# Optimization experiments

Measured on AMD Instinct MI355X. Metric: run time of the kernel, lower is better.

## Reference

```python
import jax, jax.numpy as jnp
import numpy as np

EPS = 1e-5

def conv1x1(x, w, b):
    # x: [B,Cin,H,W], w: [Cout,Cin], b: [Cout]
    return jnp.einsum('oi,bihw->bohw', w, x) + b[None, :, None, None]

def self_attention(x, qw, qb, kw, kb, vw, vb, fw, fb):
    B, C, H, W = x.shape
    hid = qw.shape[0]
    q = conv1x1(x, qw, qb).reshape(B, hid, H * W).transpose(0, 2, 1)   # [B,HW,hid]
    k = conv1x1(x, kw, kb).reshape(B, hid, H * W)                      # [B,hid,HW]
    v = conv1x1(x, vw, vb).reshape(B, C, H * W)                        # [B,C,HW]
    attn = jax.nn.softmax(jnp.einsum('bnh,bhm->bnm', q, k), axis=-1)   # [B,HW,HW]
    z = jnp.einsum('bnm,bcm->bnc', attn, v)                            # [B,HW,C]
    # faithful to torch .view(B,C,H,W) on contiguous [B,HW,C]: raw reshape, no transpose
    z = z.reshape(B, C, H, W)
    return conv1x1(z * x, fw, fb) + x

def group_norm_per_channel(y, gw, gb):
    # GroupNorm(num_groups == num_channels): per-channel instance norm, biased var
    mean = y.mean(axis=(2, 3), keepdims=True)
    var = ((y - mean) ** 2).mean(axis=(2, 3), keepdims=True)
    yn = (y - mean) * jax.lax.rsqrt(var + EPS)
    return yn * gw[None, :, None, None] + gb[None, :, None, None]

def setup_inputs() -> dict:
    key = jax.random.key(0)
    ks = jax.random.split(key, 32)
    B, C, H, W = 4, 64, 64, 64
    hid, att = 64, 64
    d = {}
    d['x'] = jax.random.normal(ks[0], (B, C, H, W), jnp.float32)
    d['h'] = jax.random.normal(ks[1], (B, hid, H, W), jnp.float32)
    d['c'] = jax.random.normal(ks[2], (B, hid, H, W), jnp.float32)
    i = 3
    for pre, cin in (('ax', C), ('ah', hid)):
        for nm, cout in (('q', att), ('k', att), ('v', cin), ('f', cin)):
            d[f'{pre}_{nm}w'] = jax.random.normal(ks[i], (cout, cin), jnp.float32) * 0.05; i += 1
            d[f'{pre}_{nm}b'] = jax.random.normal(ks[i], (cout,), jnp.float32) * 0.05; i += 1
    d['conv_w'] = jax.random.normal(ks[i], (4 * hid, C + hid, 3, 3), jnp.float32) * 0.05; i += 1
    d['conv_b'] = jax.random.normal(ks[i], (4 * hid,), jnp.float32) * 0.05; i += 1
    d['gn_w'] = jnp.ones((4 * hid,), jnp.float32)
    d['gn_b'] = jnp.zeros((4 * hid,), jnp.float32)
    return d

def reference(x, h, c,
              ax_qw, ax_qb, ax_kw, ax_kb, ax_vw, ax_vb, ax_fw, ax_fb,
              ah_qw, ah_qb, ah_kw, ah_kb, ah_vw, ah_vb, ah_fw, ah_fb,
              conv_w, conv_b, gn_w, gn_b):
    hid = h.shape[1]
    xa = self_attention(x, ax_qw, ax_qb, ax_kw, ax_kb, ax_vw, ax_vb, ax_fw, ax_fb)
    ha = self_attention(h, ah_qw, ah_qb, ah_kw, ah_kb, ah_vw, ah_vb, ah_fw, ah_fb)
    combined = jnp.concatenate([xa, ha], axis=1)
    y = jax.lax.conv_general_dilated(
        combined, conv_w, window_strides=(1, 1), padding=[(1, 1), (1, 1)],
        dimension_numbers=('NCHW', 'OIHW', 'NCHW')) + conv_b[None, :, None, None]
    y = group_norm_per_channel(y, gn_w, gn_b)
    i, f, o, g = jnp.split(y, 4, axis=1)
    i = jax.nn.sigmoid(i); f = jax.nn.sigmoid(f); o = jax.nn.sigmoid(o); g = jnp.tanh(g)
    c_next = f * c + i * g
    h_next = o * jnp.tanh(c_next)
    return jnp.stack([h_next, c_next])  # [2,B,hid,H,W]
```

## Files before the change

### kernel.cpp

```cpp
#include <hip/hip_runtime.h>
#include <hip/hip_bf16.h>


typedef __hip_bfloat16 bf16;
typedef const __hip_bfloat16* bfp;
typedef short bf16x8 __attribute__((ext_vector_type(8)));
typedef short short4v __attribute__((ext_vector_type(4)));
typedef float f32x4 __attribute__((ext_vector_type(4)));
typedef unsigned int u32x4 __attribute__((ext_vector_type(4)));

#define SM_SHIFT 12.0f

__device__ __forceinline__ float ldf(const void* p, long i, int f32) {
    return f32 ? ((const float*)p)[i]
               : __bfloat162float(((const bf16*)p)[i]);
}
__device__ __forceinline__ short f2bf(float f) {
    bf16 h = __float2bfloat16(f);
    return *reinterpret_cast<short*>(&h);
}
__device__ __forceinline__ void xbswap(unsigned& a, unsigned& b, int mask, bool up) {
    unsigned s = up ? a : b;
    unsigned r = __shfl_xor(s, mask, 64);
    a = up ? r : a;
    b = up ? b : r;
}

__device__ __forceinline__ int sniff_f32(const void* xr)
{
    int lane = threadIdx.x & 63;
    unsigned long long v = ((const unsigned long long*)xr)[lane];
    int ok = 0;
#pragma unroll
    for (int i = 0; i < 4; ++i) {
        int e = (int)((v >> (16 * i + 7)) & 0xFF);
        ok += (e >= 100 && e <= 141);
    }
    ok += __shfl_xor(ok, 1, 64);
    ok += __shfl_xor(ok, 2, 64);
    ok += __shfl_xor(ok, 4, 64);
    ok += __shfl_xor(ok, 8, 64);
    ok += __shfl_xor(ok, 16, 64);
    ok += __shfl_xor(ok, 32, 64);
    return ok < 200;
}

__global__ __launch_bounds__(256) void qkv_kernel(
    const void* __restrict__ Xx, const void* __restrict__ Xh,
    const void* __restrict__ qwx, const void* __restrict__ qbx,
    const void* __restrict__ kwx, const void* __restrict__ kbx,
    const void* __restrict__ vwx, const void* __restrict__ vbx,
    const void* __restrict__ qwh, const void* __restrict__ qbh,
    const void* __restrict__ kwh, const void* __restrict__ kbh,
    const void* __restrict__ vwh, const void* __restrict__ vbh,
    bf16* __restrict__ Qx, bf16* __restrict__ Kx, bf16* __restrict__ Vtx,
    bf16* __restrict__ Qh, bf16* __restrict__ Kh, bf16* __restrict__ Vth,
    const void* __restrict__ cw, bf16* __restrict__ Wt,
    float* __restrict__ gacc, int qkvN)
{
    int bx = blockIdx.x;
    int tid = threadIdx.x;
    int f32 = sniff_f32(Xx);
    if (bx >= qkvN) {
        if (bx == qkvN) {
            for (int j = 0; j < 8; ++j)
                gacc[tid * 8 + j] = 0.f;
        }
        int wi = (bx - qkvN) * 256 + tid;
        int tap = wi >> 15;
        int rem = wi & 32767;
        int oc = rem >> 7, ic = rem & 127;
        Wt[wi] = __float2bfloat16(ldf(cw, ((long)oc * 128 + ic) * 9 + tap, f32));
        return;
    }
    __shared__ __align__(16) short xt[64][72];
    __shared__ __align__(16) short wq[64][72];
    __shared__ __align__(16) short wk[64][72];
    __shared__ __align__(16) short wv[64][72];
    int ab  = (bx >> 8) & 1;
    int idx = bx & 255;
    int b = idx >> 6;
    int n0 = (idx & 63) * 64;
    int wave = tid >> 6, lane = tid & 63;
    int q = lane >> 4, l15 = lane & 15;

    const void* X = ab ? Xh : Xx;
    const void* qw = ab ? qwh : qwx; const void* qb = ab ? qbh : qbx;
    const void* kw = ab ? kwh : kwx; const void* kb = ab ? kbh : kbx;
    const void* vw = ab ? vwh : vwx; const void* vb = ab ? vbh : vbx;
    short* Qg  = (short*)(ab ? Qh  : Qx)  + (long)b * 262144;
    short* Kg  = (short*)(ab ? Kh  : Kx)  + (long)b * 262144;
    short* Vtg = (short*)(ab ? Vth : Vtx) + (long)b * 262144;

    if (!f32) {
        const short* q16 = (const short*)qw;
        const short* k16 = (const short*)kw;
        const short* v16 = (const short*)vw;
        for (int rep = 0; rep < 2; ++rep) {
            int j8 = (rep * 256 + tid) * 8;
            *(bf16x8*)&wq[j8 >> 6][j8 & 63] = *(const bf16x8*)(q16 + j8);
            *(bf16x8*)&wk[j8 >> 6][j8 & 63] = *(const bf16x8*)(k16 + j8);
            *(bf16x8*)&wv[j8 >> 6][j8 & 63] = *(const bf16x8*)(v16 + j8);
        }
    } else {
        for (int rep = 0; rep < 16; ++rep) {
            int j = rep * 256 + tid;
            int i = j >> 6, cc = j & 63;
            wq[i][cc] = f2bf(((const float*)qw)[j]);
            wk[i][cc] = f2bf(((const float*)kw)[j]);
            wv[i][cc] = f2bf(((const float*)vw)[j]);
        }
    }
    long xbase = (long)b * 262144;
    for (int rep = 0; rep < 16; ++rep) {
        int c = rep * 4 + (tid >> 6);
        int p = tid & 63;
        xt[p][c] = f2bf(ldf(X, xbase + (long)c * 4096 + n0 + p, f32));
    }
    __syncthreads();

    bf16x8 a0 = *(const bf16x8*)&xt[wave * 16 + l15][q * 8];
    bf16x8 a1 = *(const bf16x8*)&xt[wave * 16 + l15][32 + q * 8];

    for (int ct = 0; ct < 4; ++ct) {
        bf16x8 bq0 = *(const bf16x8*)&wq[ct * 16 + l15][q * 8];
        bf16x8 bq1 = *(const bf16x8*)&wq[ct * 16 + l15][32 + q * 8];
        f32x4 z = (f32x4){0.f, 0.f, 0.f, 0.f};
        z = __builtin_amdgcn_mfma_f32_16x16x32_bf16(a0, bq0, z, 0, 0, 0);
        z = __builtin_amdgcn_mfma_f32_16x16x32_bf16(a1, bq1, z, 0, 0, 0);
        float bias = ldf(qb, ct * 16 + l15, f32);
        for (int reg = 0; reg < 4; ++reg)
            Qg[(long)(n0 + wave * 16 + q * 4 + reg) * 64 + ct * 16 + l15] =
                f2bf(z[reg] + bias);
    }
    for (int ct = 0; ct < 4; ++ct) {
        bf16x8 bk0 = *(const bf16x8*)&wk[ct * 16 + l15][q * 8];
        bf16x8 bk1 = *(const bf16x8*)&wk[ct * 16 + l15][32 + q * 8];
        f32x4 z = (f32x4){0.f, 0.f, 0.f, 0.f};
        z = __builtin_amdgcn_mfma_f32_16x16x32_bf16(a0, bk0, z, 0, 0, 0);
        z = __builtin_amdgcn_mfma_f32_16x16x32_bf16(a1, bk1, z, 0, 0, 0);
        float bias = ldf(kb, ct * 16 + l15, f32);
        for (int reg = 0; reg < 4; ++reg)
            Kg[(long)(n0 + wave * 16 + q * 4 + reg) * 64 + ct * 16 + l15] =
                f2bf(z[reg] + bias);
    }
    bf16x8 av0 = *(const bf16x8*)&wv[wave * 16 + l15][q * 8];
    bf16x8 av1 = *(const bf16x8*)&wv[wave * 16 + l15][32 + q * 8];
    for (int ct = 0; ct < 4; ++ct) {
        bf16x8 bx0 = *(const bf16x8*)&xt[ct * 16 + l15][q * 8];
        bf16x8 bx1 = *(const bf16x8*)&xt[ct * 16 + l15][32 + q * 8];
        f32x4 z = (f32x4){0.f, 0.f, 0.f, 0.f};
        z = __builtin_amdgcn_mfma_f32_16x16x32_bf16(av0, bx0, z, 0, 0, 0);
        z = __builtin_amdgcn_mfma_f32_16x16x32_bf16(av1, bx1, z, 0, 0, 0);
        for (int reg = 0; reg < 4; ++reg) {
            int c_out = wave * 16 + q * 4 + reg;
            float bias = ldf(vb, c_out, f32);
            Vtg[(long)c_out * 4096 + n0 + ct * 16 + l15] = f2bf(z[reg] + bias);
        }
    }
}

__global__ __launch_bounds__(256, 2) void attn_kernel(
    bfp Qx, bfp Kx, bfp Vtx, bf16* Ox,
    bfp Qh, bfp Kh, bfp Vth, bf16* Oh,
    float* __restrict__ lw, int split)
{
    __shared__ __align__(16) short ks [2][64][64];
    __shared__ __align__(16) short vts[2][64][64];
    int tid = threadIdx.x;
    int wave = tid >> 6, lane = tid & 63;
    int q = lane >> 4, l15 = lane & 15;
    int idx = blockIdx.x & 255;
    int ab, half, mstart, ntile;
    if (split) {
        ab = blockIdx.x >> 9; half = (blockIdx.x >> 8) & 1;
        mstart = half * 2048; ntile = 32;
    } else {
        ab = blockIdx.x >> 8; half = 0; mstart = 0; ntile = 64;
    }
    int b = idx >> 6;
    int rt = idx & 63;
    int n0 = rt * 64 + wave * 16;
    const short* Qb  = (const short*)(ab ? Qh  : Qx)  + (long)b * 262144;
    const short* Kb  = (const short*)(ab ? Kh  : Kx)  + (long)b * 262144;
    const short* Vtb = (const short*)(ab ? Vth : Vtx) + (long)b * 262144;
    short* Ob = (short*)(ab ? Oh : Ox) + (long)half * (1l << 20) + (long)b * 262144;

    bf16x8 aq0 = *(const bf16x8*)(Qb + (long)(n0 + l15) * 64 + q * 8);
    bf16x8 aq1 = *(const bf16x8*)(Qb + (long)(n0 + l15) * 64 + 32 + q * 8);

    f32x4 acc_o[4];
    for (int ct = 0; ct < 4; ++ct) acc_o[ct] = (f32x4){0.f, 0.f, 0.f, 0.f};
    float l_acc = 0.f;

    int swp = (l15 >> 1) & 7;
    int c0 = (q ^ swp) << 3;
    int c1 = ((q + 4) ^ swp) << 3;
    int sw_s = (tid >> 4) & 7;
    int cs = (((tid & 7) ^ sw_s)) << 3;

    bool up5 = (lane & 32) != 0;
    bool up4 = (lane & 16) != 0;

    int r0 = tid >> 3, r1 = r0 + 32;
    bf16x8 pk0 = *(const bf16x8*)(Kb + (long)(mstart + r0) * 64 + (tid & 7) * 8);
    bf16x8 pk1 = *(const bf16x8*)(Kb + (long)(mstart + r1) * 64 + (tid & 7) * 8);
    bf16x8 pv0 = *(const bf16x8*)(Vtb + (long)r0 * 4096 + mstart + (tid & 7) * 8);
    bf16x8 pv1 = *(const bf16x8*)(Vtb + (long)r1 * 4096 + mstart + (tid & 7) * 8);

    for (int it = 0; it < ntile; ++it) {
        int buf = it & 1;
        *(bf16x8*)&ks[buf][r0][cs]  = pk0;
        *(bf16x8*)&ks[buf][r1][cs]  = pk1;
        *(bf16x8*)&vts[buf][r0][cs] = pv0;
        *(bf16x8*)&vts[buf][r1][cs] = pv1;
        __syncthreads();
        if (it + 1 < ntile) {
            long m = (long)mstart + (long)(it + 1) * 64;
            pk0 = *(const bf16x8*)(Kb + (m + r0) * 64 + (tid & 7) * 8);
            pk1 = *(const bf16x8*)(Kb + (m + r1) * 64 + (tid & 7) * 8);
            pv0 = *(const bf16x8*)(Vtb + (long)r0 * 4096 + m + (tid & 7) * 8);
            pv1 = *(const bf16x8*)(Vtb + (long)r1 * 4096 + m + (tid & 7) * 8);
        }

        f32x4 s[4];
#pragma unroll
        for (int t = 0; t < 4; ++t) {
            const short* krow = &ks[buf][t * 16 + l15][0];
            bf16x8 ak0 = *(const bf16x8*)(krow + c0);
            bf16x8 ak1 = *(const bf16x8*)(krow + c1);
            f32x4 z = (f32x4){0.f, 0.f, 0.f, 0.f};
            z    = __builtin_amdgcn_mfma_f32_16x16x32_bf16(ak0, aq0, z, 0, 0, 0);
            s[t] = __builtin_amdgcn_mfma_f32_16x16x32_bf16(ak1, aq1, z, 0, 0, 0);
        }

        unsigned P32[8];
        float lt = 0.f;
#pragma unroll
        for (int t = 0; t < 4; ++t) {
            float p0 = __expf(fminf(s[t][0] - SM_SHIFT, 60.f));
            float p1 = __expf(fminf(s[t][1] - SM_SHIFT, 60.f));
            float p2 = __expf(fminf(s[t][2] - SM_SHIFT, 60.f));
            float p3 = __expf(fminf(s[t][3] - SM_SHIFT, 60.f));
            lt += (p0 + p1) + (p2 + p3);
            P32[t * 2] = (unsigned)(unsigned short)f2bf(p0)
                       | ((unsigned)(unsigned short)f2bf(p1) << 16);
            P32[t * 2 + 1] = (unsigned)(unsigned short)f2bf(p2)
                           | ((unsigned)(unsigned short)f2bf(p3) << 16);
        }
        l_acc += lt;

        xbswap(P32[0], P32[2], 32, up5);
        xbswap(P32[1], P32[3], 32, up5);
        xbswap(P32[4], P32[6], 32, up5);
        xbswap(P32[5], P32[7], 32, up5);
        xbswap(P32[0], P32[2], 16, up4);
        xbswap(P32[1], P32[3], 16, up4);
        xbswap(P32[4], P32[6], 16, up4);
        xbswap(P32[5], P32[7], 16, up4);
        u32x4 B0v = (u32x4){P32[0], P32[1], P32[2], P32[3]};
        u32x4 B1v = (u32x4){P32[4], P32[5], P32[6], P32[7]};
        bf16x8 bp0 = __builtin_bit_cast(bf16x8, B0v);
        bf16x8 bp1 = __builtin_bit_cast(bf16x8, B1v);

        for (int ct = 0; ct < 4; ++ct) {
            const short* vrow = &vts[buf][ct * 16 + l15][0];
            bf16x8 av0 = *(const bf16x8*)(vrow + c0);
            bf16x8 av1 = *(const bf16x8*)(vrow + c1);
            acc_o[ct] = __builtin_amdgcn_mfma_f32_16x16x32_bf16(av0, bp0, acc_o[ct], 0, 0, 0);
            acc_o[ct] = __builtin_amdgcn_mfma_f32_16x16x32_bf16(av1, bp1, acc_o[ct], 0, 0, 0);
        }
    }

    l_acc += __shfl_xor(l_acc, 16, 64);
    l_acc += __shfl_xor(l_acc, 32, 64);

    if (split) {
        if (lane < 16) {
            lw[(long)ab * 32768 + (long)half * 16384
               + (long)b * 4096 + n0 + lane] = l_acc;
        }
        for (int ct = 0; ct < 4; ++ct) {
            short* dst = Ob + (long)(n0 + l15) * 64 + ct * 16 + q * 4;
            dst[0] = f2bf(acc_o[ct][0]);
            dst[1] = f2bf(acc_o[ct][1]);
            dst[2] = f2bf(acc_o[ct][2]);
            dst[3] = f2bf(acc_o[ct][3]);
        }
    } else {
        float iln = 1.f / l_acc;
        for (int ct = 0; ct < 4; ++ct) {
            short* dst = Ob + (long)(n0 + l15) * 64 + ct * 16 + q * 4;
            dst[0] = f2bf(acc_o[ct][0] * iln);
            dst[1] = f2bf(acc_o[ct][1] * iln);
            dst[2] = f2bf(acc_o[ct][2] * iln);
            dst[3] = f2bf(acc_o[ct][3] * iln);
        }
    }
}

__global__ __launch_bounds__(256) void attnout_kernel(
    bfp Ox, const void* __restrict__ Xx,
    const void* __restrict__ fwx, const void* __restrict__ fbx,
    bf16* __restrict__ outx,
    bfp Oh, const void* __restrict__ Xh,
    const void* __restrict__ fwh, const void* __restrict__ fbh,
    bf16* __restrict__ outh,
    const float* __restrict__ lw, int split)
{
    __shared__ __align__(16) short fwt[64][72];
    __shared__ __align__(16) short at [64][72];
    int f32 = sniff_f32(Xx);
    int ab  = blockIdx.x >> 8;
    int idx = blockIdx.x & 255;
    int b = idx >> 6;
    int h = idx & 63;
    int tid = threadIdx.x;
    int wave = tid >> 6, lane = tid & 63;
    int q = lane >> 4, l15 = lane & 15;
    bfp O = ab ? Oh : Ox;
    const void* X = ab ? Xh : Xx;
    const void* fw = ab ? fwh : fwx;
    const void* fb = ab ? fbh : fbx;
    bf16* out = ab ? outh : outx;

    if (!f32) {
        const short* f16p = (const short*)fw;
        for (int rep = 0; rep < 2; ++rep) {
            int j8 = (rep * 256 + tid) * 8;
            *(bf16x8*)&fwt[j8 >> 6][j8 & 63] = *(const bf16x8*)(f16p + j8);
        }
    } else {
        for (int rep = 0; rep < 16; ++rep) {
            int j = rep * 256 + tid;
            fwt[j >> 6][j & 63] = f2bf(((const float*)fw)[j]);
        }
    }
    const bf16* Ob0 = O + (long)b * 262144;
    const bf16* Ob1 = Ob0 + (1l << 20);
    const float* lp0 = lw + (long)ab * 32768 + (long)b * 4096;
    const float* lp1 = lp0 + 16384;
    long xbase = (long)b * 262144;
    {
        int w = tid & 63;
        for (int rep = 0; rep < 16; ++rep) {
            int cn = rep * 4 + (tid >> 6);
            int n = cn * 64 + h;
            float o;
            if (split) {
                float iln = 1.f / (lp0[n] + lp1[n]);
                o = (__bfloat162float(Ob0[(long)n * 64 + w]) +
                     __bfloat162float(Ob1[(long)n * 64 + w])) * iln;
            } else {
                o = __bfloat162float(Ob0[(long)n * 64 + w]);
            }
            float prod = o * ldf(X, xbase + (long)cn * 4096 + h * 64 + w, f32);
            at[w][cn] = f2bf(prod);
        }
    }
    __syncthreads();
    bf16x8 a0 = *(const bf16x8*)&fwt[wave * 16 + l15][q * 8];
    bf16x8 a1 = *(const bf16x8*)&fwt[wave * 16 + l15][32 + q * 8];
    short* outp = (short*)out;
    for (int nt = 0; nt < 4; ++nt) {
        bf16x8 b0 = *(const bf16x8*)&at[nt * 16 + l15][q * 8];
        bf16x8 b1 = *(const bf16x8*)&at[nt * 16 + l15][32 + q * 8];
        f32x4 z = (f32x4){0.f, 0.f, 0.f, 0.f};
        z = __builtin_amdgcn_mfma_f32_16x16x32_bf16(a0, b0, z, 0, 0, 0);
        z = __builtin_amdgcn_mfma_f32_16x16x32_bf16(a1, b1, z, 0, 0, 0);
        int w = nt * 16 + l15;
        short4v o4;
        for (int reg = 0; reg < 4; ++reg) {
            int o = wave * 16 + q * 4 + reg;
            float v = z[reg] + ldf(fb, o, f32) +
                      ldf(X, xbase + (long)o * 4096 + h * 64 + w, f32);
            o4[reg] = f2bf(v);
        }
        *(short4v*)(outp + (((long)(b * 64 + h) * 64 + w) * 64 + wave * 16 + q * 4)) = o4;
    }
}

__global__ __launch_bounds__(256) void conv3x3_kernel(
    bfp xa, bfp ha, bfp Wt, const void* __restrict__ cb,
    bf16* __restrict__ y, float* __restrict__ gacc,
    const void* __restrict__ xraw)
{
    __shared__ __align__(16) short in_s[3][66][136];
    int f32 = sniff_f32(xraw);
    int bx = blockIdx.x;
    int b = bx >> 7;
    int rem = bx & 127;
    int h = rem >> 1;
    int halfoc = rem & 1;
    int tid = threadIdx.x;
    int wave = tid >> 6, lane = tid & 63;
    int q = lane >> 4, l15 = lane & 15;

    const short* xab = (const short*)xa + (long)b * 262144;
    const short* hab = (const short*)ha + (long)b * 262144;
    const bf16x8 zv = {0, 0, 0, 0, 0, 0, 0, 0};
    for (int r = 0; r < 3; ++r) {
        int gy = h + r - 1;
        bool valid = (gy >= 0) && (gy < 64);
        for (int s = 0; s < 2; ++s) {
            int strip = s * 256 + tid;
            int w = strip >> 3;
            int c8 = (strip & 7) * 8;
            bf16x8 vx = zv, vh = zv;
            if (valid) {
                vx = *(const bf16x8*)(xab + ((long)gy * 64 + w) * 64 + c8);
                vh = *(const bf16x8*)(hab + ((long)gy * 64 + w) * 64 + c8);
            }
            *(bf16x8*)&in_s[r][w + 1][c8]      = vx;
            *(bf16x8*)&in_s[r][w + 1][64 + c8] = vh;
        }
    }
    if (tid < 96) {
        int r = tid / 32;
        int rest = tid % 32;
        int col = (rest & 1) ? 65 : 0;
        int c8 = (rest >> 1) * 8;
        *(bf16x8*)&in_s[r][col][c8] = zv;
    }
    __syncthreads();

    int oc0 = halfoc * 128 + wave * 32;
    f32x4 acc[2][4];
    for (int mt = 0; mt < 2; ++mt)
        for (int nt = 0; nt < 4; ++nt)
            acc[mt][nt] = (f32x4){0.f, 0.f, 0.f, 0.f};

    const short* Wb = (const short*)Wt;
    for (int tap = 0; tap < 9; ++tap) {
        int dy = tap / 3, dx = tap - dy * 3;
        for (int kc = 0; kc < 4; ++kc) {
            bf16x8 afrag[2];
            for (int mt = 0; mt < 2; ++mt)
                afrag[mt] = *(const bf16x8*)(
                    Wb + ((long)tap * 256 + oc0 + mt * 16 + l15) * 128 + kc * 32 + q * 8);
            for (int nt = 0; nt < 4; ++nt) {
                bf16x8 bfrag = *(const bf16x8*)&in_s[dy][nt * 16 + l15 + dx][kc * 32 + q * 8];
                for (int mt = 0; mt < 2; ++mt)
                    acc[mt][nt] = __builtin_amdgcn_mfma_f32_16x16x32_bf16(
                        afrag[mt], bfrag, acc[mt][nt], 0, 0, 0);
            }
        }
    }

    long ybase = (long)b * 1048576 + (long)h * 64;
    for (int mt = 0; mt < 2; ++mt) {
        for (int reg = 0; reg < 4; ++reg) {
            int oc = oc0 + mt * 16 + q * 4 + reg;
            float bias = ldf(cb, oc, f32);
            float s = 0.f, s2 = 0.f;
            for (int nt = 0; nt < 4; ++nt) {
                float v = acc[mt][nt][reg] + bias;
                ((short*)y)[ybase + (long)oc * 4096 + nt * 16 + l15] = f2bf(v);
                s += v; s2 = fmaf(v, v, s2);
            }
            s  += __shfl_xor(s,  1, 64);  s2 += __shfl_xor(s2, 1, 64);
            s  += __shfl_xor(s,  2, 64);  s2 += __shfl_xor(s2, 2, 64);
            s  += __shfl_xor(s,  4, 64);  s2 += __shfl_xor(s2, 4, 64);
            s  += __shfl_xor(s,  8, 64);  s2 += __shfl_xor(s2, 8, 64);
            if (l15 == 0) {
                atomicAdd(&gacc[b * 256 + oc], s);
                atomicAdd(&gacc[1024 + b * 256 + oc], s2);
            }
        }
    }
}

__global__ __launch_bounds__(256) void gates_kernel(
    bfp y, const float* __restrict__ gacc,
    const void* __restrict__ gw, const void* __restrict__ gb,
    const void* __restrict__ c_in, void* __restrict__ out)
{
    int f32 = sniff_f32(c_in);
    int idx = blockIdx.x * 256 + threadIdx.x;
    int b = idx >> 18;
    int r = idx & 262143;
    int ch = r >> 12;
    int pix = r & 4095;
    long ybase = (long)b * 1048576;
    float vals[4];
    for (int g = 0; g < 4; ++g) {
        int cc = g * 64 + ch;
        float mu  = gacc[b * 256 + cc] * (1.f / 4096.f);
        float var = gacc[1024 + b * 256 + cc] * (1.f / 4096.f) - mu * mu;
        float rstd = rsqrtf(fmaxf(var, 0.f) + 1e-5f);
        float v = __bfloat162float(y[ybase + (long)cc * 4096 + pix]);
        v = (v - mu) * rstd * ldf(gw, cc, f32) + ldf(gb, cc, f32);
        vals[g] = v;
    }
    float ig = 1.f / (1.f + __expf(-vals[0]));
    float fg = 1.f / (1.f + __expf(-vals[1]));
    float og = 1.f / (1.f + __expf(-vals[2]));
    float gg = tanhf(vals[3]);
    float cprev = ldf(c_in, idx, f32);
    float cn = fg * cprev + ig * gg;
    float hn = og * tanhf(cn);
    if (f32) {
        float* o32 = (float*)out;
        o32[idx] = hn;
        o32[1048576 + idx] = cn;
    } else {
        bf16* o16 = (bf16*)out;
        o16[idx] = __float2bfloat16(hn);
        o16[1048576 + idx] = __float2bfloat16(cn);
    }
}

extern "C" void kernel_launch(void* const* d_in, const int* in_sizes, int n_in,
                              void* d_out, int out_size, void* d_ws, size_t ws_size,
                              hipStream_t stream)
{
    const void* x = d_in[0]; const void* h = d_in[1]; const void* c = d_in[2];
    const void* ax_qw = d_in[3],  *ax_qb = d_in[4];
    const void* ax_kw = d_in[5],  *ax_kb = d_in[6];
    const void* ax_vw = d_in[7],  *ax_vb = d_in[8];
    const void* ax_fw = d_in[9],  *ax_fb = d_in[10];
    const void* ah_qw = d_in[11], *ah_qb = d_in[12];
    const void* ah_kw = d_in[13], *ah_kb = d_in[14];
    const void* ah_vw = d_in[15], *ah_vb = d_in[16];
    const void* ah_fw = d_in[17], *ah_fb = d_in[18];
    const void* conv_w = d_in[19], *conv_b = d_in[20];
    const void* gn_w = d_in[21],  *gn_b = d_in[22];

    char* wsb = (char*)d_ws;
    auto S = [&](int i) { return wsb + ((unsigned long)i << 21); };
    bool splitm = ws_size >= (27ul << 20);
    bool fused  = splitm || ws_size >= (18ul << 20) + 16384;

    bf16* ha = (bf16*)S(0);
    bf16* Wt = (bf16*)S(1);
    bf16 *Qx, *Kx, *Vtx, *Qh, *Kh, *Vth, *xa, *y, *Ox, *Oh;
    char* tail;
    if (splitm) {
        Qx = (bf16*)S(2); Kx = (bf16*)S(3); Vtx = (bf16*)S(4);
        Qh = (bf16*)S(5); Kh = (bf16*)S(6); Vth = (bf16*)S(7);
        xa = (bf16*)S(8);
        Ox = (bf16*)S(9);
        Oh = (bf16*)S(11);
        y = Qx;
        tail = S(13);
    } else if (fused) {
        Qx = (bf16*)S(2); Kx = (bf16*)S(3); Vtx = (bf16*)S(4);
        Qh = (bf16*)S(5); Kh = (bf16*)S(6); Vth = (bf16*)S(7);
        xa = (bf16*)S(8); Ox = Qx; Oh = Qh; y = Qx;
        tail = S(9);
    } else {
        Qx = (bf16*)S(2); Kx = (bf16*)S(3); Vtx = (bf16*)S(4);
        Qh = Qx; Kh = Kx; Vth = Vtx;
        xa = (bf16*)S(6); Ox = Qx; Oh = Qh; y = Qx;
        tail = S(7);
    }
    float* gacc = (float*)tail;
    float* lw   = (float*)(tail + 8192);

    if (fused) {
        qkv_kernel<<<512 + 1152, 256, 0, stream>>>(
            x, h,
            ax_qw, ax_qb, ax_kw, ax_kb, ax_vw, ax_vb,
            ah_qw, ah_qb, ah_kw, ah_kb, ah_vw, ah_vb,
            Qx, Kx, Vtx, Qh, Kh, Vth, conv_w, Wt, gacc, 512);
        if (splitm) {
            attn_kernel<<<1024, 256, 0, stream>>>(
                Qx, Kx, Vtx, Ox, Qh, Kh, Vth, Oh, lw, 1);
            attnout_kernel<<<512, 256, 0, stream>>>(
                Ox, x, ax_fw, ax_fb, xa, Oh, h, ah_fw, ah_fb, ha, lw, 1);
        } else {
            attn_kernel<<<512, 256, 0, stream>>>(
                Qx, Kx, Vtx, Ox, Qh, Kh, Vth, Oh, lw, 0);
            attnout_kernel<<<512, 256, 0, stream>>>(
                Ox, x, ax_fw, ax_fb, xa, Oh, h, ah_fw, ah_fb, ha, lw, 0);
        }
    } else {
        qkv_kernel<<<256 + 1152, 256, 0, stream>>>(
            x, x,
            ax_qw, ax_qb, ax_kw, ax_kb, ax_vw, ax_vb,
            ax_qw, ax_qb, ax_kw, ax_kb, ax_vw, ax_vb,
            Qx, Kx, Vtx, Qx, Kx, Vtx, conv_w, Wt, gacc, 256);
        attn_kernel<<<256, 256, 0, stream>>>(
            Qx, Kx, Vtx, Ox, Qx, Kx, Vtx, Ox, lw, 0);
        attnout_kernel<<<256, 256, 0, stream>>>(
            Ox, x, ax_fw, ax_fb, xa, Ox, x, ax_fw, ax_fb, xa, lw, 0);
        qkv_kernel<<<256, 256, 0, stream>>>(
            h, h,
            ah_qw, ah_qb, ah_kw, ah_kb, ah_vw, ah_vb,
            ah_qw, ah_qb, ah_kw, ah_kb, ah_vw, ah_vb,
            Qh, Kh, Vth, Qh, Kh, Vth, conv_w, Wt, gacc, 256);
        attn_kernel<<<256, 256, 0, stream>>>(
            Qh, Kh, Vth, Oh, Qh, Kh, Vth, Oh, lw, 0);
        attnout_kernel<<<256, 256, 0, stream>>>(
            Oh, h, ah_fw, ah_fb, ha, Oh, h, ah_fw, ah_fb, ha, lw, 0);
    }
    conv3x3_kernel<<<512, 256, 0, stream>>>(xa, ha, Wt, conv_b, y, gacc, x);
    gates_kernel<<<4096, 256, 0, stream>>>(y, gacc, gn_w, gn_b, c, d_out);
}
```

Baseline: 232.6 us.

## Permute K rows in LDS to drop P shuffles; use exp2 with folded shift

K tile rows are written into shared memory in a permuted order, so the S fragments from the QK MFMA come out already placed for the P·V MFMA B-operand. This removes the eight cross-lane xor shuffles per tile, and the P registers are simply regrouped into the operand vectors. The softmax exponent becomes a single fma into exp2 with the shift and clamp folded into log2-scaled constants. The risk is that the row permutation must exactly match the MFMA lane mapping, or the output is wrong.

```diff
diff --git a/kernel.cpp b/kernel.cpp
--- a/kernel.cpp
+++ b/kernel.cpp
@@ -10,6 +10,9 @@
 typedef unsigned int u32x4 __attribute__((ext_vector_type(4)));
 
 #define SM_SHIFT 12.0f
+#define LOG2E      1.4426950408889634f
+#define SM_BIAS2  -17.312340490667562f
+#define SM_CLAMP2  86.561702453337805f
 
 __device__ __forceinline__ float ldf(const void* p, long i, int f32) {
     return f32 ? ((const float*)p)[i]
@@ -18,12 +21,6 @@
 __device__ __forceinline__ short f2bf(float f) {
     bf16 h = __float2bfloat16(f);
     return *reinterpret_cast<short*>(&h);
-}
-__device__ __forceinline__ void xbswap(unsigned& a, unsigned& b, int mask, bool up) {
-    unsigned s = up ? a : b;
-    unsigned r = __shfl_xor(s, mask, 64);
-    a = up ? r : a;
-    b = up ? b : r;
 }
 
 __device__ __forceinline__ int sniff_f32(const void* xr)
@@ -199,10 +196,14 @@
     int sw_s = (tid >> 4) & 7;
     int cs = (((tid & 7) ^ sw_s)) << 3;
 
-    bool up5 = (lane & 32) != 0;
-    bool up4 = (lane & 16) != 0;
-
     int r0 = tid >> 3, r1 = r0 + 32;
+    int sr0 = (((r0 >> 5) + (((r0 >> 2) & 1) << 1)) << 4)
+            | (((r0 >> 3) & 3) << 2) | (r0 & 3);
+    int sr1 = (((r1 >> 5) + (((r1 >> 2) & 1) << 1)) << 4)
+            | (((r1 >> 3) & 3) << 2) | (r1 & 3);
+    int cs0 = (((tid & 7) ^ ((sr0 >> 1) & 7))) << 3;
+    int cs1 = (((tid & 7) ^ ((sr1 >> 1) & 7))) << 3;
+
     bf16x8 pk0 = *(const bf16x8*)(Kb + (long)(mstart + r0) * 64 + (tid & 7) * 8);
     bf16x8 pk1 = *(const bf16x8*)(Kb + (long)(mstart + r1) * 64 + (tid & 7) * 8);
     bf16x8 pv0 = *(const bf16x8*)(Vtb + (long)r0 * 4096 + mstart + (tid & 7) * 8);
@@ -210,10 +211,10 @@
 
     for (int it = 0; it < ntile; ++it) {
         int buf = it & 1;
-        *(bf16x8*)&ks[buf][r0][cs]  = pk0;
-        *(bf16x8*)&ks[buf][r1][cs]  = pk1;
-        *(bf16x8*)&vts[buf][r0][cs] = pv0;
-        *(bf16x8*)&vts[buf][r1][cs] = pv1;
+        *(bf16x8*)&ks[buf][sr0][cs0] = pk0;
+        *(bf16x8*)&ks[buf][sr1][cs1] = pk1;
+        *(bf16x8*)&vts[buf][r0][cs]  = pv0;
+        *(bf16x8*)&vts[buf][r1][cs]  = pv1;
         __syncthreads();
         if (it + 1 < ntile) {
             long m = (long)mstart + (long)(it + 1) * 64;
@@ -238,10 +239,14 @@
         float lt = 0.f;
 #pragma unroll
         for (int t = 0; t < 4; ++t) {
-            float p0 = __expf(fminf(s[t][0] - SM_SHIFT, 60.f));
-            float p1 = __expf(fminf(s[t][1] - SM_SHIFT, 60.f));
-            float p2 = __expf(fminf(s[t][2] - SM_SHIFT, 60.f));
-            float p3 = __expf(fminf(s[t][3] - SM_SHIFT, 60.f));
+            float p0 = __builtin_amdgcn_exp2f(
+                fminf(fmaf(s[t][0], LOG2E, SM_BIAS2), SM_CLAMP2));
+            float p1 = __builtin_amdgcn_exp2f(
+                fminf(fmaf(s[t][1], LOG2E, SM_BIAS2), SM_CLAMP2));
+            float p2 = __builtin_amdgcn_exp2f(
+                fminf(fmaf(s[t][2], LOG2E, SM_BIAS2), SM_CLAMP2));
+            float p3 = __builtin_amdgcn_exp2f(
+                fminf(fmaf(s[t][3], LOG2E, SM_BIAS2), SM_CLAMP2));
             lt += (p0 + p1) + (p2 + p3);
             P32[t * 2] = (unsigned)(unsigned short)f2bf(p0)
                        | ((unsigned)(unsigned short)f2bf(p1) << 16);
@@ -250,16 +255,8 @@
         }
         l_acc += lt;
 
-        xbswap(P32[0], P32[2], 32, up5);
-        xbswap(P32[1], P32[3], 32, up5);
-        xbswap(P32[4], P32[6], 32, up5);
-        xbswap(P32[5], P32[7], 32, up5);
-        xbswap(P32[0], P32[2], 16, up4);
-        xbswap(P32[1], P32[3], 16, up4);
-        xbswap(P32[4], P32[6], 16, up4);
-        xbswap(P32[5], P32[7], 16, up4);
-        u32x4 B0v = (u32x4){P32[0], P32[1], P32[2], P32[3]};
-        u32x4 B1v = (u32x4){P32[4], P32[5], P32[6], P32[7]};
+        u32x4 B0v = (u32x4){P32[0], P32[1], P32[4], P32[5]};
+        u32x4 B1v = (u32x4){P32[2], P32[3], P32[6], P32[7]};
         bf16x8 bp0 = __builtin_bit_cast(bf16x8, B0v);
         bf16x8 bp1 = __builtin_bit_cast(bf16x8, B1v);
 
```

Result: faster. 222.8 us (-4.2%).
